# Performance work log

Measured on AMD Instinct MI355X. Metric: run time of the kernel, lower is better.

Reference implementation:

```python
import math
import jax, jax.numpy as jnp
from jax import lax
import numpy as np

B, T, IN_DIM = 64, 448, 64
D, H, L, FF, K = 256, 8, 4, 1024, 3
SCALES = (1, 2, 4)
EPS = 1e-5


def _ln(x, g, b):
    m = x.mean(-1, keepdims=True)
    v = ((x - m) ** 2).mean(-1, keepdims=True)
    return (x - m) / jnp.sqrt(v + EPS) * g + b


def setup_inputs() -> dict:
    key = jax.random.key(0)
    ks = iter(jax.random.split(key, 40))
    rn = lambda shape, s=0.05: jax.random.normal(next(ks), shape, dtype=jnp.float32) * s
    S = len(SCALES)
    inp = {
        "x": jax.random.normal(next(ks), (B, T, IN_DIM), dtype=jnp.float32),
        "input_proj_w": rn((IN_DIM, D)), "input_proj_b": rn((D,)),
        "conv_w": rn((S, D, D, K)), "conv_b": rn((S, D)),
        "bn_g": jnp.ones((S, D), jnp.float32), "bn_b": jnp.zeros((S, D), jnp.float32),
        "bn_rm": jnp.zeros((S, D), jnp.float32), "bn_rv": jnp.ones((S, D), jnp.float32),
        "gate_w": rn((S * D, S)), "gate_b": rn((S,)),
        "ms_proj_w": rn((D, D)), "ms_proj_b": rn((D,)),
        "cls_token": rn((1, 1, D), 0.02),
        "qkv_w": rn((L, D, 3 * D)), "qkv_b": rn((L, 3 * D)),
        "out_w": rn((L, D, D)), "out_b": rn((L, D)),
        "alpha": jnp.full((L, H), 0.1, jnp.float32),
        "ln1_g": jnp.ones((L, D), jnp.float32), "ln1_b": jnp.zeros((L, D), jnp.float32),
        "ln2_g": jnp.ones((L, D), jnp.float32), "ln2_b": jnp.zeros((L, D), jnp.float32),
        "ffn_w1": rn((L, D, FF)), "ffn_b1": rn((L, FF)),
        "ffn_w2": rn((L, FF, D)), "ffn_b2": rn((L, D)),
        "final_g": jnp.ones((D,), jnp.float32), "final_b": jnp.zeros((D,), jnp.float32),
        "cls_w1": rn((D, D)), "cls_b1": rn((D,)),
        "cls_w2": rn((D, 1)), "cls_b2": rn((1,)),
    }
    return inp


def reference(x, input_proj_w, input_proj_b, conv_w, conv_b, bn_g, bn_b, bn_rm, bn_rv,
              gate_w, gate_b, ms_proj_w, ms_proj_b, cls_token, qkv_w, qkv_b, out_w, out_b,
              alpha, ln1_g, ln1_b, ln2_g, ln2_b, ffn_w1, ffn_b1, ffn_w2, ffn_b2,
              final_g, final_b, cls_w1, cls_b1, cls_w2, cls_b2):
    b, t, _ = x.shape
    hd = D // H
    h = x @ input_proj_w + input_proj_b  # (B,T,D)

    # multi-scale causal conv block (eval-mode batchnorm)
    xt = h.transpose(0, 2, 1)  # (B,D,T)
    outs = []
    for s, dil in enumerate(SCALES):
        pad = (K - 1) * dil
        c = lax.conv_general_dilated(xt, conv_w[s], (1,), [(pad, 0)], rhs_dilation=(dil,),
                                     dimension_numbers=("NCH", "OIH", "NCH"))
        c = c + conv_b[s][None, :, None]
        c = jax.nn.gelu(c, approximate=False)
        c = (c - bn_rm[s][None, :, None]) / jnp.sqrt(bn_rv[s][None, :, None] + EPS)
        c = c * bn_g[s][None, :, None] + bn_b[s][None, :, None]
        outs.append(c.transpose(0, 2, 1))  # (B,T,D)
    stacked = jnp.stack(outs, axis=2)  # (B,T,S,D)
    concat = jnp.concatenate(outs, axis=-1)  # (B,T,S*D)
    gate = jax.nn.softmax(concat @ gate_w + gate_b, axis=-1)[..., None]  # (B,T,S,1)
    fused = (stacked * gate).sum(axis=2)
    h = fused @ ms_proj_w + ms_proj_b + h

    # sinusoidal positional encoding
    pos = jnp.arange(t, dtype=jnp.float32)[:, None]
    div = jnp.exp(jnp.arange(0, D, 2, dtype=jnp.float32) * (-math.log(10000.0) / D))
    pe = jnp.zeros((t, D), jnp.float32)
    pe = pe.at[:, 0::2].set(jnp.sin(pos * div)).at[:, 1::2].set(jnp.cos(pos * div))
    h = h + pe[None]

    # prepend CLS
    h = jnp.concatenate([jnp.broadcast_to(cls_token, (b, 1, D)), h], axis=1)
    tt = t + 1
    dist = jnp.abs(jnp.arange(tt, dtype=jnp.float32)[:, None] - jnp.arange(tt, dtype=jnp.float32)[None, :])
    scale = math.sqrt(hd)

    for l in range(L):
        n = _ln(h, ln1_g[l], ln1_b[l])
        qkv = (n @ qkv_w[l] + qkv_b[l]).reshape(b, tt, 3, H, hd).transpose(2, 0, 3, 1, 4)
        q, k, v = qkv[0], qkv[1], qkv[2]  # (B,H,T,hd)
        logits = jnp.einsum("bhqd,bhkd->bhqk", q, k) / scale
        a = jax.nn.softplus(alpha[l])  # (H,)
        logits = logits - a[None, :, None, None] * dist
        w = jax.nn.softmax(logits, axis=-1)
        o = jnp.einsum("bhqk,bhkd->bhqd", w, v).transpose(0, 2, 1, 3).reshape(b, tt, D)
        h = h + o @ out_w[l] + out_b[l]
        n2 = _ln(h, ln2_g[l], ln2_b[l])
        f = jax.nn.gelu(n2 @ ffn_w1[l] + ffn_b1[l], approximate=False) @ ffn_w2[l] + ffn_b2[l]
        h = h + f

    h = _ln(h, final_g, final_b)
    c = h[:, 0]
    c = jax.nn.gelu(c @ cls_w1 + cls_b1, approximate=False)
    logits_out = (c @ cls_w2 + cls_b2).squeeze(-1)  # (B,)
    return logits_out
```

## Files before the change

kernel.cpp:

```cpp
#include <hip/hip_runtime.h>
#include <hip/hip_bf16.h>
#include <math.h>

#define BB   64
#define TT   448
#define TTT  449
#define DIM  256
#define HEADS 8
#define HD   32
#define LAYERS 4
#define FFD  1024
#define INDIM 64
#define MPAD 28800
#define TFRONT 160
#define MFRONT (BB*TFRONT)
#define GROWS  168

typedef __attribute__((ext_vector_type(8))) short short8;
typedef __attribute__((ext_vector_type(4))) float f32x4;
typedef unsigned short ushort_t;

__device__ __forceinline__ float gelu_f(float x) {
    float x2 = x * x;
    float m = 0.10295219f * x2 + 2.3022635f;
    float t = exp2f(-x * m);
    return x * (1.f / (1.f + t));
}
__device__ __forceinline__ ushort_t f2bf(float x) {
    unsigned u; __builtin_memcpy(&u, &x, 4);
    return (ushort_t)((u + 0x8000u) >> 16);
}
__device__ __forceinline__ unsigned pack2bf(float a, float b) {
    unsigned ua, ub;
    __builtin_memcpy(&ua, &a, 4); __builtin_memcpy(&ub, &b, 4);
    return ((ua + 0x8000u) >> 16) | ((ub + 0x8000u) & 0xffff0000u);
}
__device__ __forceinline__ float bf2f(ushort_t u) {
    unsigned v = ((unsigned)u) << 16; float f; __builtin_memcpy(&f, &v, 4); return f;
}
__device__ __forceinline__ void gload16(const ushort_t* g, ushort_t* l) {
    __builtin_amdgcn_global_load_lds(
        (const __attribute__((address_space(1))) void*)g,
        (__attribute__((address_space(3))) void*)l, 16, 0, 0);
}

__global__ __launch_bounds__(256, 3) void gemm_bf16(
    const ushort_t* __restrict__ A, const ushort_t* __restrict__ Bt,
    void* __restrict__ C, ushort_t* __restrict__ C2,
    const float* __restrict__ bias,
    const float* __restrict__ scalev, const float* __restrict__ shiftv,
    const float* __restrict__ R,
    int M, int N, int K, int a_dil, int do_gelu, int out_mode, int pe_mode,
    int rc_mod)
{
    __shared__ ushort_t smem[2 * 128 * 64];
    ushort_t* As = smem;
    ushort_t* Bs = smem + 128 * 64;
    const int tid = threadIdx.x;
    const int lane = tid & 63, w = tid >> 6;
    const int wm = w >> 1, wn = w & 1;
    const int l15 = lane & 15, quad = lane >> 4;
    const int m0 = blockIdx.y * 128, n0 = blockIdx.x * 128;
    const int sr = lane >> 3, ss = lane & 7;
    const int gsw = ss ^ sr;

    if (a_dil == -1) {
        int z = blockIdx.z;
        a_dil = 1 << z;
        Bt += (size_t)z * 196608;
        C = (void*)((ushort_t*)C + (size_t)z * MFRONT * 256);
        bias += z * 256; scalev += z * 256; shiftv += z * 256;
    }
    const ushort_t* aconv[4];
    if (a_dil > 0) {
        #pragma unroll
        for (int j = 0; j < 4; ++j) {
            int r = (w * 4 + j) * 8 + sr;
            int gm = m0 + r;
            int b = gm / TFRONT, t = gm - b * TFRONT;
            aconv[j] = A + ((size_t)(b * GROWS + 8 + t)) * 256 + gsw * 8;
        }
    }
    f32x4 acc[4][4] = {};

    for (int k0 = 0; k0 < K; k0 += 64) {
        if (a_dil > 0) {
            int tap = k0 >> 8;
            int aoff = (k0 & 255) - ((2 - tap) * a_dil) * 256;
            #pragma unroll
            for (int j = 0; j < 4; ++j)
                gload16(aconv[j] + aoff, &As[(w * 4 + j) * 512]);
        } else if (a_dil == -2) {
            const float* Af = (const float*)A;
            #pragma unroll
            for (int j = 0; j < 4; ++j) {
                int r = (w * 4 + j) * 8 + sr;
                int gm = m0 + r;
                int b = gm / TFRONT, t = gm - b * TFRONT;
                const float* ap = Af + ((size_t)b * 448 + t) * K + k0 + gsw * 8;
                float4 a0 = *(const float4*)ap;
                float4 a1 = *(const float4*)(ap + 4);
                uint2 lo = make_uint2(pack2bf(a0.x, a0.y), pack2bf(a0.z, a0.w));
                uint2 hi = make_uint2(pack2bf(a1.x, a1.y), pack2bf(a1.z, a1.w));
                *(uint2*)&As[r * 64 + ss * 8] = lo;
                *(uint2*)&As[r * 64 + ss * 8 + 4] = hi;
            }
        } else {
            #pragma unroll
            for (int j = 0; j < 4; ++j) {
                int r = (w * 4 + j) * 8 + sr;
                int g = ss ^ (r & 7);
                gload16(&A[(size_t)(m0 + r) * K + k0 + g * 8], &As[(w * 4 + j) * 512]);
            }
        }
        #pragma unroll
        for (int j = 0; j < 4; ++j) {
            int r = (w * 4 + j) * 8 + sr;
            int g = ss ^ (r & 7);
            gload16(&Bt[(size_t)(n0 + r) * K + k0 + g * 8], &Bs[(w * 4 + j) * 512]);
        }
        __syncthreads();
        #pragma unroll
        for (int ks = 0; ks < 2; ++ks) {
            short8 af[4], bfr[4];
            #pragma unroll
            for (int i = 0; i < 4; ++i) {
                int row = wm * 64 + i * 16 + l15;
                af[i] = *(const short8*)&As[row * 64 + (((ks * 4 + quad) ^ (l15 & 7)) * 8)];
            }
            #pragma unroll
            for (int j = 0; j < 4; ++j) {
                int row = wn * 64 + j * 16 + l15;
                bfr[j] = *(const short8*)&Bs[row * 64 + (((ks * 4 + quad) ^ (l15 & 7)) * 8)];
            }
            #pragma unroll
            for (int i = 0; i < 4; ++i)
                #pragma unroll
                for (int j = 0; j < 4; ++j)
                    acc[i][j] = __builtin_amdgcn_mfma_f32_16x16x32_bf16(
                        af[i], bfr[j], acc[i][j], 0, 0, 0);
        }
        __syncthreads();
    }

    float* wreg = (float*)smem + w * 2048;
    const int gn0 = n0 + wn * 64 + l15 * 4;
    float4 bias4 = bias ? *(const float4*)&bias[gn0] : make_float4(0.f, 0.f, 0.f, 0.f);
    float4 scl4, shf4;
    if (scalev) { scl4 = *(const float4*)&scalev[gn0]; shf4 = *(const float4*)&shiftv[gn0]; }
    else        { scl4 = make_float4(1.f, 1.f, 1.f, 1.f); shf4 = make_float4(0.f, 0.f, 0.f, 0.f); }

    #pragma unroll
    for (int ci = 0; ci < 2; ++ci) {
        #pragma unroll
        for (int i2 = 0; i2 < 2; ++i2) {
            int i = ci * 2 + i2;
            #pragma unroll
            for (int j = 0; j < 4; ++j) {
                float* col = &wreg[(i2 * 16 + quad * 4) * 64 + j * 16 + l15];
                #pragma unroll
                for (int r = 0; r < 4; ++r) col[r * 64] = acc[i][j][r];
            }
        }
        #pragma unroll
        for (int rr = 0; rr < 8; ++rr) {
            int rl = rr * 4 + quad;
            float4 v = *(float4*)&wreg[rl * 64 + l15 * 4];
            int gm = m0 + wm * 64 + ci * 32 + rl;
            v.x += bias4.x; v.y += bias4.y; v.z += bias4.z; v.w += bias4.w;
            if (do_gelu) { v.x = gelu_f(v.x); v.y = gelu_f(v.y); v.z = gelu_f(v.z); v.w = gelu_f(v.w); }
            v.x = v.x * scl4.x + shf4.x; v.y = v.y * scl4.y + shf4.y;
            v.z = v.z * scl4.z + shf4.z; v.w = v.w * scl4.w + shf4.w;
            size_t crow = (size_t)gm;
            if (rc_mod > 0) crow = (size_t)(gm / rc_mod) * 449 + (gm % rc_mod);
            if (R) {
                float4 r4 = *(const float4*)&R[crow * N + gn0];
                v.x += r4.x; v.y += r4.y; v.z += r4.z; v.w += r4.w;
            }
            if (pe_mode) {
                int bi = gm / TFRONT, t = gm - bi * TFRONT;
                float ft = (float)t;
                float f0 = __expf(-9.210340371976184f * (float)gn0 * (1.f / 256.f));
                float f1 = __expf(-9.210340371976184f * (float)(gn0 + 2) * (1.f / 256.f));
                float a0 = ft * f0, a1 = ft * f1;
                v.x += __sinf(a0); v.y += __cosf(a0);
                v.z += __sinf(a1); v.w += __cosf(a1);
                *(float4*)&((float*)C)[(size_t)(bi * 449 + 1 + t) * 256 + gn0] = v;
            } else if (out_mode == 1) {
                uint2 pk = make_uint2(pack2bf(v.x, v.y), pack2bf(v.z, v.w));
                *(uint2*)&((ushort_t*)C)[crow * N + gn0] = pk;
            } else {
                *(float4*)&((float*)C)[crow * N + gn0] = v;
                if (out_mode == 2) {
                    int bi = gm / TFRONT, t = gm - bi * TFRONT;
                    size_t grow = (size_t)(bi * GROWS + 8 + t);
                    uint2 pk = make_uint2(pack2bf(v.x, v.y), pack2bf(v.z, v.w));
                    *(uint2*)&C2[grow * N + gn0] = pk;
                }
            }
        }
    }
}

__global__ __launch_bounds__(256) void prep_all(
    const float* __restrict__ ipw,  const float* __restrict__ mpw,
    const float* __restrict__ qkvw, const float* __restrict__ outw,
    const float* __restrict__ fw1,  const float* __restrict__ fw2,
    const float* __restrict__ cw1,
    ushort_t* ipwT, ushort_t* mpwT, ushort_t* qkvT, ushort_t* outwT,
    ushort_t* fw1T, ushort_t* fw2T, ushort_t* cw1T,
    const float* __restrict__ convw, ushort_t* wrepT,
    const float* __restrict__ bg, const float* __restrict__ bb,
    const float* __restrict__ rm, const float* __restrict__ rv,
    float* bnsc, float* bnsh,
    ushort_t* h448g, const float* __restrict__ clstok, float* h449)
{
    const int bid = blockIdx.x;
    if (bid >= 3175) {
        int b = bid - 3175;
        h449[(size_t)b * TTT * 256 + threadIdx.x] = clstok[threadIdx.x];
        return;
    }
    if (bid >= 3111) {
        int b = bid - 3111;
        #pragma unroll
        for (int j = 0; j < 8; ++j)
            h448g[(size_t)(b * GROWS + j) * 256 + threadIdx.x] = 0;
        return;
    }
    if (bid >= 3108) {
        int i = (bid - 3108) * 256 + threadIdx.x;
        if (i < 768) {
            float sc = rsqrtf(rv[i] + 1e-5f) * bg[i];
            bnsc[i] = sc;
            bnsh[i] = bb[i] - rm[i] * sc;
        }
        return;
    }
    if (bid >= 804) {
        int i = (bid - 804) * 256 + threadIdx.x;
        int s = i / 196608; int o = i - s * 196608;
        int ci = o & 255; int t3 = (o >> 8) % 3; int co = o / 768;
        wrepT[i] = f2bf(convw[(((size_t)s * 256 + co) * 256 + ci) * 3 + t3]);
        return;
    }
    const float* src; ushort_t* dst; int K, N, local;
    if (bid < 4)        { src = ipw;  dst = ipwT;  K = 64;   N = 256;  local = bid; }
    else if (bid < 20)  { src = mpw;  dst = mpwT;  K = 256;  N = 256;  local = bid - 4; }
    else if (bid < 212) { int l = bid - 20;  int z = l / 48; l -= z * 48;
                          src = qkvw + (size_t)z * 196608; dst = qkvT + (size_t)z * 196608;
                          K = 256;  N = 768;  local = l; }
    else if (bid < 276) { int l = bid - 212; int z = l / 16; l -= z * 16;
                          src = outw + (size_t)z * 65536;  dst = outwT + (size_t)z * 65536;
                          K = 256;  N = 256;  local = l; }
    else if (bid < 532) { int l = bid - 276; int z = l / 64; l -= z * 64;
                          src = fw1 + (size_t)z * 262144;  dst = fw1T + (size_t)z * 262144;
                          K = 256;  N = 1024; local = l; }
    else if (bid < 788) { int l = bid - 532; int z = l / 64; l -= z * 64;
                          src = fw2 + (size_t)z * 262144;  dst = fw2T + (size_t)z * 262144;
                          K = 1024; N = 256;  local = l; }
    else                { src = cw1;  dst = cw1T;  K = 256;  N = 256;  local = bid - 788; }

    __shared__ float tile[64][65];
    int nt = N / 64;
    int n0 = (local % nt) * 64, k0 = (local / nt) * 64;
    int tx = threadIdx.x & 63, ty = threadIdx.x >> 6;
    #pragma unroll
    for (int i = 0; i < 16; ++i)
        tile[i * 4 + ty][tx] = src[(size_t)(k0 + i * 4 + ty) * N + n0 + tx];
    __syncthreads();
    #pragma unroll
    for (int i = 0; i < 16; ++i) {
        int n = i * 4 + ty;
        dst[(size_t)(n0 + n) * K + k0 + tx] = f2bf(tile[tx][n]);
    }
}

__global__ __launch_bounds__(256) void gate_fuse(
    const ushort_t* __restrict__ conv,
    const float* __restrict__ gw, const float* __restrict__ gb,
    ushort_t* __restrict__ fused, int Mrows)
{
    const int w = threadIdx.x >> 6, lane = threadIdx.x & 63;
    const int m = blockIdx.x * 4 + w;
    const int d0 = lane * 4;
    float vals[3][4];
    float p0 = 0.f, p1 = 0.f, p2 = 0.f;
    #pragma unroll
    for (int s = 0; s < 3; ++s) {
        uint2 pk = *(const uint2*)&conv[((size_t)s * Mrows + m) * 256 + d0];
        vals[s][0] = bf2f(pk.x & 0xffff); vals[s][1] = bf2f(pk.x >> 16);
        vals[s][2] = bf2f(pk.y & 0xffff); vals[s][3] = bf2f(pk.y >> 16);
        #pragma unroll
        for (int e = 0; e < 4; ++e) {
            const float* wp = gw + (size_t)(s * 256 + d0 + e) * 3;
            float v = vals[s][e];
            p0 += v * wp[0]; p1 += v * wp[1]; p2 += v * wp[2];
        }
    }
    #pragma unroll
    for (int o = 32; o > 0; o >>= 1) {
        p0 += __shfl_xor(p0, o); p1 += __shfl_xor(p1, o); p2 += __shfl_xor(p2, o);
    }
    float l0 = p0 + gb[0], l1 = p1 + gb[1], l2 = p2 + gb[2];
    float mx = fmaxf(l0, fmaxf(l1, l2));
    float e0 = __expf(l0 - mx), e1 = __expf(l1 - mx), e2 = __expf(l2 - mx);
    float inv = 1.f / (e0 + e1 + e2);
    float g0 = e0 * inv, g1 = e1 * inv, g2 = e2 * inv;
    unsigned r0 = pack2bf(vals[0][0] * g0 + vals[1][0] * g1 + vals[2][0] * g2,
                          vals[0][1] * g0 + vals[1][1] * g1 + vals[2][1] * g2);
    unsigned r1 = pack2bf(vals[0][2] * g0 + vals[1][2] * g1 + vals[2][2] * g2,
                          vals[0][3] * g0 + vals[1][3] * g1 + vals[2][3] * g2);
    *(uint2*)&fused[(size_t)m * 256 + d0] = make_uint2(r0, r1);
}

__global__ __launch_bounds__(256) void ln_rows8(
    const float* __restrict__ X, ushort_t* __restrict__ Y,
    const float* __restrict__ g, const float* __restrict__ b,
    int xmod, int nrows)
{
    const int w = threadIdx.x >> 6, lane = threadIdx.x & 63;
    const int row0 = blockIdx.x * 8 + w * 2;
    if (row0 >= nrows) return;
    const int d0 = lane * 4;
    const bool two = (row0 + 1) < nrows;
    size_t xr0 = (size_t)(row0 / xmod) * 449 + (row0 % xmod);
    int row1 = row0 + 1;
    size_t xr1 = two ? (size_t)(row1 / xmod) * 449 + (row1 % xmod) : xr0;
    float4 va = *(const float4*)&X[xr0 * 256 + d0];
    float4 vb = *(const float4*)&X[xr1 * 256 + d0];
    float sa = va.x + va.y + va.z + va.w;
    float sb = vb.x + vb.y + vb.z + vb.w;
    #pragma unroll
    for (int o = 32; o > 0; o >>= 1) { sa += __shfl_xor(sa, o); sb += __shfl_xor(sb, o); }
    float ma = sa * (1.f / 256.f), mb = sb * (1.f / 256.f);
    float ax = va.x - ma, ay = va.y - ma, az = va.z - ma, aw = va.w - ma;
    float bx = vb.x - mb, by = vb.y - mb, bz = vb.z - mb, bw = vb.w - mb;
    float s2a = ax * ax + ay * ay + az * az + aw * aw;
    float s2b = bx * bx + by * by + bz * bz + bw * bw;
    #pragma unroll
    for (int o = 32; o > 0; o >>= 1) { s2a += __shfl_xor(s2a, o); s2b += __shfl_xor(s2b, o); }
    float ia = rsqrtf(s2a * (1.f / 256.f) + 1e-5f);
    float ib = rsqrtf(s2b * (1.f / 256.f) + 1e-5f);
    float4 gv = *(const float4*)&g[d0];
    float4 bv = *(const float4*)&b[d0];
    *(uint2*)&Y[(size_t)row0 * 256 + d0] = make_uint2(
        pack2bf(ax * ia * gv.x + bv.x, ay * ia * gv.y + bv.y),
        pack2bf(az * ia * gv.z + bv.z, aw * ia * gv.w + bv.w));
    if (two)
        *(uint2*)&Y[(size_t)row1 * 256 + d0] = make_uint2(
            pack2bf(bx * ib * gv.x + bv.x, by * ib * gv.y + bv.y),
            pack2bf(bz * ib * gv.z + bv.z, bw * ib * gv.w + bv.w));
}

#define KP    480
#define KPAD  36
#define VPAD  488
#define PTPAD 40
__global__ __launch_bounds__(256, 2) void attn8_kernel(
    const ushort_t* __restrict__ qkv,
    const float* __restrict__ alpha,
    ushort_t* __restrict__ O,
    int kst, int nqt, int ost)
{
    __shared__ ushort_t sK[KP][KPAD];
    __shared__ ushort_t sVt[32][VPAD];
    __shared__ ushort_t sPT[4][16][PTPAD];
    __shared__ float sRed[4];

    const int bh = blockIdx.x;
    const int b = bh >> 3, h = bh & 7;
    const int tid = threadIdx.x;
    const int w = tid >> 6, lane = tid & 63;
    const int l15 = lane & 15, quad = lane >> 4;
    const float LOG2E = 1.4426950408889634f;
    const float scale2 = 0.17677669529663687f * LOG2E;

    float av = alpha[h];
    float a_sp = (av > 20.f) ? av : log1pf(__expf(av));
    const float a_h = a_sp * LOG2E;

    {
        int r0 = tid >> 2, c = (tid & 3) * 8;
        float knmax = 0.f;
        for (int r = r0; r < kst; r += 64) {
            const ushort_t* src = qkv + ((size_t)(b * kst + r)) * 768 + 256 + h * 32 + c;
            short8 kv = *(const short8*)src;
            short8 vv = *(const short8*)(src + 256);
            *(short8*)&sK[r][c] = kv;
            float ssq = 0.f;
            #pragma unroll
            for (int j = 0; j < 8; ++j) {
                float kf = bf2f(((const ushort_t*)&kv)[j]);
                ssq += kf * kf;
                sVt[c + j][r] = ((const ushort_t*)&vv)[j];
            }
            ssq += __shfl_xor(ssq, 1);
            ssq += __shfl_xor(ssq, 2);
            knmax = fmaxf(knmax, ssq);
        }
        #pragma unroll
        for (int o = 32; o > 0; o >>= 1) knmax = fmaxf(knmax, __shfl_xor(knmax, o));
        if (lane == 0) sRed[w] = knmax;
    }
    __syncthreads();
    const float kmax2 = fmaxf(fmaxf(sRed[0], sRed[1]), fmaxf(sRed[2], sRed[3]));

    for (int qt = w; qt < nqt; qt += 4) {
        const int qb = qt * 16;
        const int qrow = qb + l15;
        short8 qfrag = *(const short8*)(qkv + ((size_t)(b * kst + qrow)) * 768 + h * 32 + quad * 8);
        const f32x4 z = {0.f, 0.f, 0.f, 0.f};

        float qn = 0.f;
        #pragma unroll
        for (int j = 0; j < 8; ++j) { float f = bf2f(qfrag[j]); qn += f * f; }
        qn += __shfl_xor(qn, 16);
        qn += __shfl_xor(qn, 32);
        const float Mr = scale2 * sqrtf(qn * kmax2);
        const float fq = (float)qrow;

        int ch_lo = (qb - 32) >> 5; if (ch_lo < 0) ch_lo = 0;
        int ch_hi = (qb + 47) >> 5;
        const int ch_max = (kst >> 5) - 1;
        if (ch_hi > ch_max) ch_hi = ch_max;

        f32x4 o0 = z, o1 = z;
        float lsum = 0.f;
        for (int ch = ch_lo; ch <= ch_hi; ++ch) {
            const int kb = ch * 32;
            short8 kf0 = *(const short8*)&sK[kb + l15][quad * 8];
            short8 kf1 = *(const short8*)&sK[kb + 16 + l15][quad * 8];
            f32x4 s0 = __builtin_amdgcn_mfma_f32_16x16x32_bf16(kf0, qfrag, z, 0, 0, 0);
            f32x4 s1 = __builtin_amdgcn_mfma_f32_16x16x32_bf16(kf1, qfrag, z, 0, 0, 0);
            float p0[4], p1[4];
            #pragma unroll
            for (int r = 0; r < 4; ++r) {
                int k0 = kb + quad * 4 + r;
                int k1 = k0 + 16;
                float b0 = s0[r] * scale2 - (a_h * fabsf(fq - (float)k0) + Mr);
                float b1 = s1[r] * scale2 - (a_h * fabsf(fq - (float)k1) + Mr);
                p0[r] = exp2f(b0);
                p1[r] = exp2f(b1);
            }
            lsum += (p0[0] + p0[1]) + (p0[2] + p0[3]) + (p1[0] + p1[1]) + (p1[2] + p1[3]);
            unsigned* prow = (unsigned*)&sPT[w][l15][0];
            prow[quad * 2]     = pack2bf(p0[0], p0[1]);
            prow[quad * 2 + 1] = pack2bf(p0[2], p0[3]);
            prow[8 + quad * 2]     = pack2bf(p1[0], p1[1]);
            prow[8 + quad * 2 + 1] = pack2bf(p1[2], p1[3]);
            short8 pB = *(const short8*)&sPT[w][l15][quad * 8];
            short8 v0 = *(const short8*)&sVt[l15][kb + quad * 8];
            short8 v1 = *(const short8*)&sVt[16 + l15][kb + quad * 8];
            o0 = __builtin_amdgcn_mfma_f32_16x16x32_bf16(v0, pB, o0, 0, 0, 0);
            o1 = __builtin_amdgcn_mfma_f32_16x16x32_bf16(v1, pB, o1, 0, 0, 0);
        }
        lsum += __shfl_xor(lsum, 16);
        lsum += __shfl_xor(lsum, 32);

        {
            float inv = 1.f / lsum;
            unsigned* dst = (unsigned*)&O[((size_t)(b * ost + qrow)) * 256 + h * 32 + quad * 4];
            dst[0] = pack2bf(o0[0] * inv, o0[1] * inv);
            dst[1] = pack2bf(o0[2] * inv, o0[3] * inv);
            dst[8] = pack2bf(o1[0] * inv, o1[1] * inv);
            dst[9] = pack2bf(o1[2] * inv, o1[3] * inv);
        }
    }
}

__global__ __launch_bounds__(256) void head_kernel(
    const float* __restrict__ h449,
    const float* __restrict__ fing, const float* __restrict__ finb,
    const ushort_t* __restrict__ cw1T, const float* __restrict__ cb1,
    const float* __restrict__ cw2, const float* __restrict__ b2,
    float* __restrict__ out)
{
    __shared__ float xn[256];
    __shared__ float red[4];
    const int b = blockIdx.x, d = threadIdx.x;
    float v = h449[(size_t)b * TTT * 256 + d];
    float s = v;
    #pragma unroll
    for (int o = 32; o > 0; o >>= 1) s += __shfl_down(s, o, 64);
    if ((d & 63) == 0) red[d >> 6] = s;
    __syncthreads();
    float mean = (red[0] + red[1] + red[2] + red[3]) * (1.f / 256.f);
    __syncthreads();
    float diff = v - mean;
    float s2 = diff * diff;
    #pragma unroll
    for (int o = 32; o > 0; o >>= 1) s2 += __shfl_down(s2, o, 64);
    if ((d & 63) == 0) red[d >> 6] = s2;
    __syncthreads();
    float rstd = rsqrtf((red[0] + red[1] + red[2] + red[3]) * (1.f / 256.f) + 1e-5f);
    xn[d] = diff * rstd * fing[d] + finb[d];
    __syncthreads();
    const ushort_t* wrow = cw1T + (size_t)d * 256;
    float acc = 0.f;
    #pragma unroll 4
    for (int k = 0; k < 256; k += 8) {
        short8 wv = *(const short8*)&wrow[k];
        #pragma unroll
        for (int j = 0; j < 8; ++j) acc += xn[k + j] * bf2f(((const ushort_t*)&wv)[j]);
    }
    float p = gelu_f(acc + cb1[d]) * cw2[d];
    #pragma unroll
    for (int o = 32; o > 0; o >>= 1) p += __shfl_down(p, o, 64);
    __syncthreads();
    if ((d & 63) == 0) red[d >> 6] = p;
    __syncthreads();
    if (d == 0) out[b] = red[0] + red[1] + red[2] + red[3] + b2[0];
}

extern "C" void kernel_launch(void* const* d_in, const int* in_sizes, int n_in,
                              void* d_out, int out_size, void* d_ws, size_t ws_size,
                              hipStream_t stream)
{
    const float* x      = (const float*)d_in[0];
    const float* ipw    = (const float*)d_in[1];
    const float* ipb    = (const float*)d_in[2];
    const float* convw  = (const float*)d_in[3];
    const float* convb  = (const float*)d_in[4];
    const float* bng    = (const float*)d_in[5];
    const float* bnb    = (const float*)d_in[6];
    const float* bnrm   = (const float*)d_in[7];
    const float* bnrv   = (const float*)d_in[8];
    const float* gatew  = (const float*)d_in[9];
    const float* gateb  = (const float*)d_in[10];
    const float* mpw    = (const float*)d_in[11];
    const float* mpb    = (const float*)d_in[12];
    const float* clstok = (const float*)d_in[13];
    const float* qkvw   = (const float*)d_in[14];
    const float* qkvb   = (const float*)d_in[15];
    const float* outw   = (const float*)d_in[16];
    const float* outb   = (const float*)d_in[17];
    const float* alpha  = (const float*)d_in[18];
    const float* ln1g   = (const float*)d_in[19];
    const float* ln1b   = (const float*)d_in[20];
    const float* ln2g   = (const float*)d_in[21];
    const float* ln2b   = (const float*)d_in[22];
    const float* fw1    = (const float*)d_in[23];
    const float* fb1    = (const float*)d_in[24];
    const float* fw2    = (const float*)d_in[25];
    const float* fb2    = (const float*)d_in[26];
    const float* fing   = (const float*)d_in[27];
    const float* finb   = (const float*)d_in[28];
    const float* cw1    = (const float*)d_in[29];
    const float* cb1    = (const float*)d_in[30];
    const float* cw2    = (const float*)d_in[31];
    const float* cb2    = (const float*)d_in[32];

    const int KL[4] = {160, 128, 96, 64};
    const int QL[4] = {128, 96, 64, 16};

    char* base = (char*)d_ws;
    size_t off = 0;
    auto alloc = [&](size_t bytes) { char* p = base + off; off += (bytes + 255) & ~(size_t)255; return p; };
    float*    h448  = (float*)alloc((size_t)MFRONT * 256 * 4);
    float*    h449  = (float*)alloc((size_t)MPAD * 256 * 4);
    float*    bufA  = (float*)alloc((size_t)MFRONT * 768 * 4);
    ushort_t* conv_bf = (ushort_t*)bufA;
    ushort_t* qkv_bf  = (ushort_t*)bufA;
    ushort_t* bufMid  = (ushort_t*)bufA;
    ushort_t* bufB  = (ushort_t*)alloc((size_t)MFRONT * 256 * 2);
    ushort_t* bufB2 = (ushort_t*)alloc((size_t)MFRONT * 256 * 2);
    ushort_t* bufC  = (ushort_t*)alloc((size_t)64 * 128 * 256 * 2);
    ushort_t* h448g = (ushort_t*)alloc((size_t)BB * GROWS * 256 * 2);
    ushort_t* wrepT = (ushort_t*)alloc((size_t)3 * 256 * 768 * 2);
    ushort_t* ipwT  = (ushort_t*)alloc((size_t)64 * 256 * 2);
    ushort_t* mpwT  = (ushort_t*)alloc((size_t)256 * 256 * 2);
    ushort_t* qkvT  = (ushort_t*)alloc((size_t)4 * 768 * 256 * 2);
    ushort_t* outwT = (ushort_t*)alloc((size_t)4 * 256 * 256 * 2);
    ushort_t* fw1T  = (ushort_t*)alloc((size_t)4 * 1024 * 256 * 2);
    ushort_t* fw2T  = (ushort_t*)alloc((size_t)4 * 256 * 1024 * 2);
    ushort_t* cw1T  = (ushort_t*)alloc((size_t)256 * 256 * 2);
    float*    bnsc  = (float*)alloc(768 * 4);
    float*    bnsh  = (float*)alloc(768 * 4);

    auto gemm = [&](const ushort_t* A, const ushort_t* Bt, void* C, ushort_t* C2,
                    const float* bias, const float* scl, const float* shf, const float* R,
                    int M, int N, int K, int a_dil, int gelu_fl, int omode, int pemode,
                    int rc_mod = 0, int gz = 1) {
        dim3 grid(N / 128, M / 128, gz);
        hipLaunchKernelGGL(gemm_bf16, grid, dim3(256), 0, stream,
                           A, Bt, C, C2, bias, scl, shf, R, M, N, K, a_dil, gelu_fl,
                           omode, pemode, rc_mod);
    };

    hipLaunchKernelGGL(prep_all, dim3(3239), dim3(256), 0, stream,
                       ipw, mpw, qkvw, outw, fw1, fw2, cw1,
                       ipwT, mpwT, qkvT, outwT, fw1T, fw2T, cw1T,
                       convw, wrepT, bng, bnb, bnrm, bnrv, bnsc, bnsh,
                       h448g, clstok, h449);

    gemm((const ushort_t*)x, ipwT, h448, h448g, ipb, nullptr, nullptr, nullptr,
         MFRONT, 256, 64, -2, 0, 2, 0);

    gemm(h448g, wrepT, conv_bf, nullptr, convb, bnsc, bnsh, nullptr,
         MFRONT, 256, 768, -1, 1, 1, 0, 0, 3);
    hipLaunchKernelGGL(gate_fuse, dim3(MFRONT / 4), dim3(256), 0, stream,
                       conv_bf, gatew, gateb, bufB, MFRONT);
    gemm(bufB, mpwT, h449, nullptr, mpb, nullptr, nullptr, h448,
         MFRONT, 256, 256, 0, 0, 0, 1);

    for (int l = 0; l < LAYERS; ++l) {
        const int Kl = KL[l], Ql = QL[l];
        const int MK = 64 * Kl, MQ = 64 * Ql;
        hipLaunchKernelGGL(ln_rows8, dim3((MK + 7) / 8), dim3(256), 0, stream,
                           h449, bufB2, ln1g + l * 256, ln1b + l * 256, Kl, MK);
        gemm(bufB2, qkvT + (size_t)l * 768 * 256, qkv_bf, nullptr, qkvb + l * 768,
             nullptr, nullptr, nullptr, MK, 768, 256, 0, 0, 1, 0);
        hipLaunchKernelGGL(attn8_kernel, dim3(BB * HEADS), dim3(256), 0, stream,
                           qkv_bf, alpha + l * HEADS, bufC, Kl, Ql / 16, Ql);
        gemm(bufC, outwT + (size_t)l * 65536, h449, nullptr, outb + l * 256,
             nullptr, nullptr, h449, MQ, 256, 256, 0, 0, 0, 0, Ql);
        hipLaunchKernelGGL(ln_rows8, dim3((MQ + 7) / 8), dim3(256), 0, stream,
                           h449, bufB2, ln2g + l * 256, ln2b + l * 256, Ql, MQ);
        gemm(bufB2, fw1T + (size_t)l * 262144, bufMid, nullptr, fb1 + l * 1024,
             nullptr, nullptr, nullptr, MQ, 1024, 256, 0, 1, 1, 0);
        gemm(bufMid, fw2T + (size_t)l * 262144, h449, nullptr, fb2 + l * 256,
             nullptr, nullptr, h449, MQ, 256, 1024, 0, 0, 0, 0, Ql);
    }

    hipLaunchKernelGGL(head_kernel, dim3(BB), dim3(256), 0, stream,
                       h449, fing, finb, cw1T, cb1, cw2, cb2, (float*)d_out);
}
```

Measured before the change: 533.1 us.

## Fuse LayerNorm into GEMM epilogues with full-row tiles

Adds a gemm_ln kernel that computes a 64x256 output tile, so each block holds complete rows. It applies bias, residual and optional positional encoding, then computes the row LayerNorm through shared-memory reductions and writes both the fp32 residual stream and the bf16 normalized input for the next GEMM. This removes every standalone ln_rows8 launch and the extra read of the residual stream that each one did. The CLS-row LN1 is precomputed in prep_all. In exchange, the full-row tiles and the several block-wide barriers in the epilogue may reduce occupancy or parallelism for the smaller M sizes.

```diff
diff --git a/kernel.cpp b/kernel.cpp
--- a/kernel.cpp
+++ b/kernel.cpp
@@ -202,6 +202,159 @@
     }
 }
 
+__global__ __launch_bounds__(256, 3) void gemm_ln(
+    const ushort_t* __restrict__ A, const ushort_t* __restrict__ Bt,
+    float* __restrict__ C, ushort_t* __restrict__ Y,
+    const float* __restrict__ bias, const float* __restrict__ R,
+    const float* __restrict__ lng, const float* __restrict__ lnb,
+    int M, int K, int pe_mode, int rc_mod)
+{
+    __shared__ __align__(16) char smraw[42240];
+    ushort_t* As = (ushort_t*)smraw;
+    ushort_t* Bs = (ushort_t*)(smraw + 8192);
+    float* sums = (float*)(smraw + 40960);
+    float* sqs  = (float*)(smraw + 41472);
+    float* mst  = (float*)(smraw + 41984);
+    const int tid = threadIdx.x;
+    const int lane = tid & 63, w = tid >> 6;
+    const int l15 = lane & 15, quad = lane >> 4;
+    const int m0 = blockIdx.y * 64;
+    const int sr = lane >> 3, ss = lane & 7;
+    const int gsw = ss ^ sr;
+
+    f32x4 acc[4][4] = {};
+
+    for (int k0 = 0; k0 < K; k0 += 64) {
+        #pragma unroll
+        for (int j = 0; j < 2; ++j) {
+            int ch = w * 2 + j;
+            gload16(&A[(size_t)(m0 + ch * 8 + sr) * K + k0 + gsw * 8], &As[ch * 512]);
+        }
+        #pragma unroll
+        for (int j = 0; j < 8; ++j) {
+            int ch = w * 8 + j;
+            gload16(&Bt[(size_t)(ch * 8 + sr) * K + k0 + gsw * 8], &Bs[ch * 512]);
+        }
+        __syncthreads();
+        #pragma unroll
+        for (int ks = 0; ks < 2; ++ks) {
+            short8 af[4], bfr[4];
+            #pragma unroll
+            for (int i = 0; i < 4; ++i) {
+                int row = i * 16 + l15;
+                af[i] = *(const short8*)&As[row * 64 + (((ks * 4 + quad) ^ (l15 & 7)) * 8)];
+            }
+            #pragma unroll
+            for (int j = 0; j < 4; ++j) {
+                int row = w * 64 + j * 16 + l15;
+                bfr[j] = *(const short8*)&Bs[row * 64 + (((ks * 4 + quad) ^ (l15 & 7)) * 8)];
+            }
+            #pragma unroll
+            for (int i = 0; i < 4; ++i)
+                #pragma unroll
+                for (int j = 0; j < 4; ++j)
+                    acc[i][j] = __builtin_amdgcn_mfma_f32_16x16x32_bf16(
+                        af[i], bfr[j], acc[i][j], 0, 0, 0);
+        }
+        __syncthreads();
+    }
+
+    float* wreg = (float*)smraw + w * 2048;
+    const int gn0 = w * 64 + l15 * 4;
+    float4 bias4 = *(const float4*)&bias[gn0];
+    float4 g4 = make_float4(0.f, 0.f, 0.f, 0.f), b4 = g4;
+    if (Y) { g4 = *(const float4*)&lng[gn0]; b4 = *(const float4*)&lnb[gn0]; }
+
+    #pragma unroll
+    for (int ci = 0; ci < 2; ++ci) {
+        #pragma unroll
+        for (int i2 = 0; i2 < 2; ++i2) {
+            int i = ci * 2 + i2;
+            #pragma unroll
+            for (int j = 0; j < 4; ++j) {
+                float* col = &wreg[(i2 * 16 + quad * 4) * 64 + j * 16 + l15];
+                #pragma unroll
+                for (int r = 0; r < 4; ++r) col[r * 64] = acc[i][j][r];
+            }
+        }
+        #pragma unroll
+        for (int rr = 0; rr < 8; ++rr) {
+            int rl = rr * 4 + quad;
+            int gm = m0 + ci * 32 + rl;
+            float4 v = *(float4*)&wreg[rl * 64 + l15 * 4];
+            v.x += bias4.x; v.y += bias4.y; v.z += bias4.z; v.w += bias4.w;
+            size_t crow = (size_t)gm;
+            if (rc_mod > 0) crow = (size_t)(gm / rc_mod) * 449 + (gm % rc_mod);
+            if (R) {
+                float4 r4 = *(const float4*)&R[crow * 256 + gn0];
+                v.x += r4.x; v.y += r4.y; v.z += r4.z; v.w += r4.w;
+            }
+            if (pe_mode) {
+                int bi = gm / TFRONT, t = gm - bi * TFRONT;
+                float ft = (float)t;
+                float f0 = __expf(-9.210340371976184f * (float)gn0 * (1.f / 256.f));
+                float f1 = __expf(-9.210340371976184f * (float)(gn0 + 2) * (1.f / 256.f));
+                float a0 = ft * f0, a1 = ft * f1;
+                v.x += __sinf(a0); v.y += __cosf(a0);
+                v.z += __sinf(a1); v.w += __cosf(a1);
+            }
+            *(float4*)&wreg[rl * 64 + l15 * 4] = v;
+            float s = (v.x + v.y) + (v.z + v.w);
+            s += __shfl_xor(s, 1); s += __shfl_xor(s, 2);
+            s += __shfl_xor(s, 4); s += __shfl_xor(s, 8);
+            if (l15 == 0) sums[rl * 4 + w] = s;
+        }
+        __syncthreads();
+        if (tid < 32)
+            mst[tid] = (sums[tid * 4] + sums[tid * 4 + 1] +
+                        sums[tid * 4 + 2] + sums[tid * 4 + 3]) * (1.f / 256.f);
+        __syncthreads();
+        #pragma unroll
+        for (int rr = 0; rr < 8; ++rr) {
+            int rl = rr * 4 + quad;
+            float4 v = *(float4*)&wreg[rl * 64 + l15 * 4];
+            float m = mst[rl];
+            float dx = v.x - m, dy = v.y - m, dz = v.z - m, dw = v.w - m;
+            float s2 = (dx * dx + dy * dy) + (dz * dz + dw * dw);
+            s2 += __shfl_xor(s2, 1); s2 += __shfl_xor(s2, 2);
+            s2 += __shfl_xor(s2, 4); s2 += __shfl_xor(s2, 8);
+            if (l15 == 0) sqs[rl * 4 + w] = s2;
+        }
+        __syncthreads();
+        if (tid < 32)
+            mst[32 + tid] = rsqrtf((sqs[tid * 4] + sqs[tid * 4 + 1] +
+                                    sqs[tid * 4 + 2] + sqs[tid * 4 + 3]) * (1.f / 256.f) + 1e-5f);
+        __syncthreads();
+        #pragma unroll
+        for (int rr = 0; rr < 8; ++rr) {
+            int rl = rr * 4 + quad;
+            int gm = m0 + ci * 32 + rl;
+            float4 v = *(float4*)&wreg[rl * 64 + l15 * 4];
+            if (pe_mode) {
+                int bi = gm / TFRONT, t = gm - bi * TFRONT;
+                *(float4*)&C[(size_t)(bi * 449 + 1 + t) * 256 + gn0] = v;
+                if (Y && t != TFRONT - 1) {
+                    float m = mst[rl], rs = mst[32 + rl];
+                    *(uint2*)&Y[(size_t)(gm + 1) * 256 + gn0] = make_uint2(
+                        pack2bf((v.x - m) * rs * g4.x + b4.x, (v.y - m) * rs * g4.y + b4.y),
+                        pack2bf((v.z - m) * rs * g4.z + b4.z, (v.w - m) * rs * g4.w + b4.w));
+                }
+            } else {
+                size_t crow = (size_t)gm;
+                if (rc_mod > 0) crow = (size_t)(gm / rc_mod) * 449 + (gm % rc_mod);
+                *(float4*)&C[crow * 256 + gn0] = v;
+                if (Y) {
+                    float m = mst[rl], rs = mst[32 + rl];
+                    *(uint2*)&Y[(size_t)gm * 256 + gn0] = make_uint2(
+                        pack2bf((v.x - m) * rs * g4.x + b4.x, (v.y - m) * rs * g4.y + b4.y),
+                        pack2bf((v.z - m) * rs * g4.z + b4.z, (v.w - m) * rs * g4.w + b4.w));
+                }
+            }
+        }
+        __syncthreads();
+    }
+}
+
 __global__ __launch_bounds__(256) void prep_all(
     const float* __restrict__ ipw,  const float* __restrict__ mpw,
     const float* __restrict__ qkvw, const float* __restrict__ outw,
@@ -213,9 +366,34 @@
     const float* __restrict__ bg, const float* __restrict__ bb,
     const float* __restrict__ rm, const float* __restrict__ rv,
     float* bnsc, float* bnsh,
-    ushort_t* h448g, const float* __restrict__ clstok, float* h449)
+    ushort_t* h448g, const float* __restrict__ clstok, float* h449,
+    const float* __restrict__ ln1g0, const float* __restrict__ ln1b0,
+    ushort_t* clsY)
 {
+    __shared__ float redp[4];
     const int bid = blockIdx.x;
+    if (bid >= 3239) {
+        const int d = threadIdx.x;
+        float v = clstok[d];
+        float s = v;
+        #pragma unroll
+        for (int o = 32; o > 0; o >>= 1) s += __shfl_down(s, o, 64);
+        if ((d & 63) == 0) redp[d >> 6] = s;
+        __syncthreads();
+        float mean = (redp[0] + redp[1] + redp[2] + redp[3]) * (1.f / 256.f);
+        __syncthreads();
+        float diff = v - mean;
+        float s2 = diff * diff;
+        #pragma unroll
+        for (int o = 32; o > 0; o >>= 1) s2 += __shfl_down(s2, o, 64);
+        if ((d & 63) == 0) redp[d >> 6] = s2;
+        __syncthreads();
+        float rstd = rsqrtf((redp[0] + redp[1] + redp[2] + redp[3]) * (1.f / 256.f) + 1e-5f);
+        ushort_t y = f2bf(diff * rstd * ln1g0[d] + ln1b0[d]);
+        for (int b = 0; b < BB; ++b)
+            clsY[(size_t)(b * TFRONT) * 256 + d] = y;
+        return;
+    }
     if (bid >= 3175) {
         int b = bid - 3175;
         h449[(size_t)b * TTT * 256 + threadIdx.x] = clstok[threadIdx.x];
@@ -312,45 +490,6 @@
     unsigned r1 = pack2bf(vals[0][2] * g0 + vals[1][2] * g1 + vals[2][2] * g2,
                           vals[0][3] * g0 + vals[1][3] * g1 + vals[2][3] * g2);
     *(uint2*)&fused[(size_t)m * 256 + d0] = make_uint2(r0, r1);
-}
-
-__global__ __launch_bounds__(256) void ln_rows8(
-    const float* __restrict__ X, ushort_t* __restrict__ Y,
-    const float* __restrict__ g, const float* __restrict__ b,
-    int xmod, int nrows)
-{
-    const int w = threadIdx.x >> 6, lane = threadIdx.x & 63;
-    const int row0 = blockIdx.x * 8 + w * 2;
-    if (row0 >= nrows) return;
-    const int d0 = lane * 4;
-    const bool two = (row0 + 1) < nrows;
-    size_t xr0 = (size_t)(row0 / xmod) * 449 + (row0 % xmod);
-    int row1 = row0 + 1;
-    size_t xr1 = two ? (size_t)(row1 / xmod) * 449 + (row1 % xmod) : xr0;
-    float4 va = *(const float4*)&X[xr0 * 256 + d0];
-    float4 vb = *(const float4*)&X[xr1 * 256 + d0];
-    float sa = va.x + va.y + va.z + va.w;
-    float sb = vb.x + vb.y + vb.z + vb.w;
-    #pragma unroll
-    for (int o = 32; o > 0; o >>= 1) { sa += __shfl_xor(sa, o); sb += __shfl_xor(sb, o); }
-    float ma = sa * (1.f / 256.f), mb = sb * (1.f / 256.f);
-    float ax = va.x - ma, ay = va.y - ma, az = va.z - ma, aw = va.w - ma;
-    float bx = vb.x - mb, by = vb.y - mb, bz = vb.z - mb, bw = vb.w - mb;
-    float s2a = ax * ax + ay * ay + az * az + aw * aw;
-    float s2b = bx * bx + by * by + bz * bz + bw * bw;
-    #pragma unroll
-    for (int o = 32; o > 0; o >>= 1) { s2a += __shfl_xor(s2a, o); s2b += __shfl_xor(s2b, o); }
-    float ia = rsqrtf(s2a * (1.f / 256.f) + 1e-5f);
-    float ib = rsqrtf(s2b * (1.f / 256.f) + 1e-5f);
-    float4 gv = *(const float4*)&g[d0];
-    float4 bv = *(const float4*)&b[d0];
-    *(uint2*)&Y[(size_t)row0 * 256 + d0] = make_uint2(
-        pack2bf(ax * ia * gv.x + bv.x, ay * ia * gv.y + bv.y),
-        pack2bf(az * ia * gv.z + bv.z, aw * ia * gv.w + bv.w));
-    if (two)
-        *(uint2*)&Y[(size_t)row1 * 256 + d0] = make_uint2(
-            pack2bf(bx * ib * gv.x + bv.x, by * ib * gv.y + bv.y),
-            pack2bf(bz * ib * gv.z + bv.z, bw * ib * gv.w + bv.w));
 }
 
 #define KP    480
@@ -587,12 +726,19 @@
                            A, Bt, C, C2, bias, scl, shf, R, M, N, K, a_dil, gelu_fl,
                            omode, pemode, rc_mod);
     };
-
-    hipLaunchKernelGGL(prep_all, dim3(3239), dim3(256), 0, stream,
+    auto gemmln = [&](const ushort_t* A, const ushort_t* Bt, float* C, ushort_t* Yp,
+                      const float* bias, const float* R,
+                      const float* g, const float* b,
+                      int M, int K, int pemode, int rcm) {
+        hipLaunchKernelGGL(gemm_ln, dim3(1, M / 64), dim3(256), 0, stream,
+                           A, Bt, C, Yp, bias, R, g, b, M, K, pemode, rcm);
+    };
+
+    hipLaunchKernelGGL(prep_all, dim3(3240), dim3(256), 0, stream,
                        ipw, mpw, qkvw, outw, fw1, fw2, cw1,
                        ipwT, mpwT, qkvT, outwT, fw1T, fw2T, cw1T,
                        convw, wrepT, bng, bnb, bnrm, bnrv, bnsc, bnsh,
-                       h448g, clstok, h449);
+                       h448g, clstok, h449, ln1g, ln1b, bufB2);
 
     gemm((const ushort_t*)x, ipwT, h448, h448g, ipb, nullptr, nullptr, nullptr,
          MFRONT, 256, 64, -2, 0, 2, 0);
@@ -601,26 +747,25 @@
          MFRONT, 256, 768, -1, 1, 1, 0, 0, 3);
     hipLaunchKernelGGL(gate_fuse, dim3(MFRONT / 4), dim3(256), 0, stream,
                        conv_bf, gatew, gateb, bufB, MFRONT);
-    gemm(bufB, mpwT, h449, nullptr, mpb, nullptr, nullptr, h448,
-         MFRONT, 256, 256, 0, 0, 0, 1);
+    gemmln(bufB, mpwT, h449, bufB2, mpb, h448, ln1g, ln1b,
+           MFRONT, 256, 1, 0);
 
     for (int l = 0; l < LAYERS; ++l) {
         const int Kl = KL[l], Ql = QL[l];
         const int MK = 64 * Kl, MQ = 64 * Ql;
-        hipLaunchKernelGGL(ln_rows8, dim3((MK + 7) / 8), dim3(256), 0, stream,
-                           h449, bufB2, ln1g + l * 256, ln1b + l * 256, Kl, MK);
         gemm(bufB2, qkvT + (size_t)l * 768 * 256, qkv_bf, nullptr, qkvb + l * 768,
              nullptr, nullptr, nullptr, MK, 768, 256, 0, 0, 1, 0);
         hipLaunchKernelGGL(attn8_kernel, dim3(BB * HEADS), dim3(256), 0, stream,
                            qkv_bf, alpha + l * HEADS, bufC, Kl, Ql / 16, Ql);
-        gemm(bufC, outwT + (size_t)l * 65536, h449, nullptr, outb + l * 256,
-             nullptr, nullptr, h449, MQ, 256, 256, 0, 0, 0, 0, Ql);
-        hipLaunchKernelGGL(ln_rows8, dim3((MQ + 7) / 8), dim3(256), 0, stream,
-                           h449, bufB2, ln2g + l * 256, ln2b + l * 256, Ql, MQ);
+        gemmln(bufC, outwT + (size_t)l * 65536, h449, bufB2, outb + l * 256,
+               h449, ln2g + l * 256, ln2b + l * 256, MQ, 256, 0, Ql);
         gemm(bufB2, fw1T + (size_t)l * 262144, bufMid, nullptr, fb1 + l * 1024,
              nullptr, nullptr, nullptr, MQ, 1024, 256, 0, 1, 1, 0);
-        gemm(bufMid, fw2T + (size_t)l * 262144, h449, nullptr, fb2 + l * 256,
-             nullptr, nullptr, h449, MQ, 256, 1024, 0, 0, 0, 0, Ql);
+        gemmln(bufMid, fw2T + (size_t)l * 262144, h449,
+               (l < 3) ? bufB2 : nullptr, fb2 + l * 256, h449,
+               (l < 3) ? ln1g + (l + 1) * 256 : nullptr,
+               (l < 3) ? ln1b + (l + 1) * 256 : nullptr,
+               MQ, 1024, 0, Ql);
     }
 
     hipLaunchKernelGGL(head_kernel, dim3(BB), dim3(256), 0, stream,
```

Result: slower. 583.7 us (+9.5%).
